# Kernel tuning notes

Hardware: AMD Instinct MI355X
Metric: run time of the kernel (lower is better)

The kernel has to match this reference:

```python
import jax, jax.numpy as jnp
import numpy as np

M = 4  # mixture size of the AttentionStem value embedding

def unfold_windows(a, kh, kw, Hout, Wout):
    # a: [..., Hp, Wp] -> [..., Hout, Wout, kh, kw] (stride-1 sliding windows, cropped)
    rows = []
    for i in range(kh):
        cols = [a[..., i:i + Hout, j:j + Wout] for j in range(kw)]
        rows.append(jnp.stack(cols, axis=-1))
    return jnp.stack(rows, axis=-2)

def attention_stem(x, qw, kw_, vw, emb_a, emb_b, emb_mix, kh, kw, pad):
    # x: [B,Cin,H,W]; qw/kw_: [Cin,Co]; vw: [M,Cin,Co]; emb_a:[Co,kh]; emb_b:[Co,kw]; emb_mix:[M,Co]
    B, Cin, H, W = x.shape
    pl, pr, pt, pb = pad  # F.pad order (left,right,top,bottom)
    xp = jnp.pad(x, ((0, 0), (0, 0), (pt, pb), (pl, pr)))
    Hp, Wp = xp.shape[2], xp.shape[3]
    Hout = min(Hp - kh + 1, H)
    Wout = min(Wp - kw + 1, W)
    q = jnp.einsum('bchw,co->bohw', x[:, :, :Hout, :Wout], qw)       # 1x1 conv query
    k = jnp.einsum('bchw,co->bohw', xp, kw_)                          # 1x1 conv key on padded
    v = jnp.einsum('bchw,mco->mbohw', xp, vw)                         # m 1x1 conv values
    k_win = unfold_windows(k, kh, kw, Hout, Wout)                     # [B,Co,Ho,Wo,kh,kw]
    v_win = unfold_windows(v, kh, kw, Hout, Wout)                     # [M,B,Co,Ho,Wo,kh,kw]
    # mixture relative-position embedding, softmax over mixtures per (kh,kw) offset
    la = emb_mix @ emb_a                                              # [M,kh]
    lb = emb_mix @ emb_b                                              # [M,kw]
    emb = jax.nn.softmax(la[:, :, None] + lb[:, None, :], axis=0)     # [M,kh,kw]
    v_agg = jnp.einsum('mkl,mbohwkl->bohwkl', emb, v_win)             # [B,Co,Ho,Wo,kh,kw]
    K = kh * kw
    scores = jnp.einsum('bohw,bohwkl->bhwkl', q, k_win).reshape(B, Hout, Wout, K)
    attn = jax.nn.softmax(scores, axis=-1).reshape(B, Hout, Wout, kh, kw)
    out = jnp.einsum('bhwkl,bohwkl->bohw', attn, v_agg)               # [B,Co,Ho,Wo]
    return out

def bn_relu(x, g, b):
    # training-mode BatchNorm2d + ReLU
    mu = x.mean(axis=(0, 2, 3), keepdims=True)
    var = x.var(axis=(0, 2, 3), keepdims=True)
    y = (x - mu) * jax.lax.rsqrt(var + 1e-5) * g[None, :, None, None] + b[None, :, None, None]
    return jax.nn.relu(y)

def _params(key):
    ks = jax.random.split(key, 18)
    def w(k, shape):
        return jax.random.normal(k, shape, dtype=jnp.float32) * 0.1
    cfg = [(1, 64, 1, 5), (64, 128, 2, 5), (128, 16, 2, 5)]
    p = {}
    i = 0
    for s, (ci, co, kh, kw) in enumerate(cfg):
        p[f'p{s}_q'] = w(ks[i], (ci, co)); i += 1
        p[f'p{s}_k'] = w(ks[i], (ci, co)); i += 1
        p[f'p{s}_v'] = w(ks[i], (M, ci, co)); i += 1
        p[f'p{s}_ea'] = w(ks[i], (co, kh)); i += 1
        p[f'p{s}_eb'] = w(ks[i], (co, kw)); i += 1
        p[f'p{s}_em'] = w(ks[i], (M, co)); i += 1
        p[f'p{s}_g'] = jnp.ones((co,), jnp.float32)
        p[f'p{s}_b'] = jnp.zeros((co,), jnp.float32)
    return p

def setup_inputs() -> dict:
    key = jax.random.key(0)
    kx, kp = jax.random.split(key)
    inp = {'x': jax.random.normal(kx, (2, 1, 8, 3000), dtype=jnp.float32)}
    inp.update(_params(kp))
    return inp

def reference(x,
              p0_q, p0_k, p0_v, p0_ea, p0_eb, p0_em, p0_g, p0_b,
              p1_q, p1_k, p1_v, p1_ea, p1_eb, p1_em, p1_g, p1_b,
              p2_q, p2_k, p2_v, p2_ea, p2_eb, p2_em, p2_g, p2_b):
    h = attention_stem(x, p0_q, p0_k, p0_v, p0_ea, p0_eb, p0_em, 1, 5, (2, 2, 0, 0))
    h = bn_relu(h, p0_g, p0_b)[:, :, ::2, ::2]                        # MaxPool2d(1,2) == stride-2 subsample
    h = attention_stem(h, p1_q, p1_k, p1_v, p1_ea, p1_eb, p1_em, 2, 5, (2, 2, 1, 1))
    h = bn_relu(h, p1_g, p1_b)[:, :, ::2, ::2]
    h = attention_stem(h, p2_q, p2_k, p2_v, p2_ea, p2_eb, p2_em, 2, 5, (2, 2, 0, 0))
    h = bn_relu(h, p2_g, p2_b)
    B, C, H, W = h.shape
    nW = W // 56                                                       # AvgPool2d((1,56))
    return h[:, :, :, :nW * 56].reshape(B, C, H, nW, 56).mean(-1)
```

## Files before the change

### kernel.cpp

```cpp
#include <hip/hip_runtime.h>
#include <math.h>


#define TPB 256

__global__ void stage0_kernel(const float* __restrict__ x,
                              const float* __restrict__ qw0, const float* __restrict__ kw0,
                              const float* __restrict__ vw0, const float* __restrict__ ea0,
                              const float* __restrict__ eb0, const float* __restrict__ em0,
                              const float* __restrict__ qw1, const float* __restrict__ kw1,
                              const float* __restrict__ vw1, const float* __restrict__ ea1,
                              const float* __restrict__ eb1, const float* __restrict__ em1,
                              const float* __restrict__ qw2, const float* __restrict__ kw2,
                              const float* __restrict__ vw2, const float* __restrict__ ea2,
                              const float* __restrict__ eb2, const float* __restrict__ em2,
                              float* __restrict__ h0raw,
                              float2* __restrict__ part0,
                              float* __restrict__ G,
                              float* __restrict__ Wy,
                              float* __restrict__ embs1g,
                              float* __restrict__ Wcat2) {
    int tid = threadIdx.x;
    int bx = blockIdx.x;
    if (bx >= 94) {
        if (blockIdx.y != 0 || blockIdx.z != 0) return;
        int role = bx - 94;
        __shared__ float la[8], lb[20], embs[40];
        if (role == 0) {
            if (tid < 8) {
                int m = tid / 2, k = tid % 2;
                float s = 0.f;
                for (int o = 0; o < 128; ++o) s += em1[m * 128 + o] * ea1[o * 2 + k];
                la[tid] = s;
            }
            if (tid >= 64 && tid < 84) {
                int r = tid - 64;
                int m = r / 5, l = r % 5;
                float s = 0.f;
                for (int o = 0; o < 128; ++o) s += em1[m * 128 + o] * eb1[o * 5 + l];
                lb[r] = s;
            }
            __syncthreads();
            if (tid < 10) {
                int k = tid / 5, l = tid % 5;
                float lg[4], mx = -1e30f;
                for (int m = 0; m < 4; ++m) {
                    lg[m] = la[m * 2 + k] + lb[m * 5 + l];
                    mx = fmaxf(mx, lg[m]);
                }
                float sum = 0.f;
                for (int m = 0; m < 4; ++m) { lg[m] = expf(lg[m] - mx); sum += lg[m]; }
                float inv = 1.f / sum;
                for (int m = 0; m < 4; ++m) embs[tid * 4 + m] = lg[m] * inv;
            }
            __syncthreads();
            if (tid < 40) embs1g[tid] = embs[tid];
            for (int e = tid; e < 2048; e += 256) {
                int c = e >> 6, c2 = e & 63;
                float s = 0.f;
                for (int o = 0; o < 128; ++o)
                    s = fmaf(qw1[c * 128 + o], kw1[c2 * 128 + o], s);
                G[e] = s;
            }
        } else if (role == 1) {
            for (int e = 2048 + tid; e < 4096; e += 256) {
                int c = e >> 6, c2 = e & 63;
                float s = 0.f;
                for (int o = 0; o < 128; ++o)
                    s = fmaf(qw1[c * 128 + o], kw1[c2 * 128 + o], s);
                G[e] = s;
            }
        } else if (role == 2 || role == 3) {
            int base = (role - 2) * 16384;
            for (int e = base + tid; e < base + 16384; e += 256) {
                int r = e >> 6, c = e & 63;
                int m = r >> 7, o = r & 127;
                Wy[e] = vw1[(m * 64 + c) * 128 + o];
            }
        } else {
            if (tid < 8) {
                int m = tid / 2, k = tid % 2;
                float s = 0.f;
                for (int o = 0; o < 16; ++o) s += em2[m * 16 + o] * ea2[o * 2 + k];
                la[tid] = s;
            }
            if (tid >= 64 && tid < 84) {
                int r = tid - 64;
                int m = r / 5, l = r % 5;
                float s = 0.f;
                for (int o = 0; o < 16; ++o) s += em2[m * 16 + o] * eb2[o * 5 + l];
                lb[r] = s;
            }
            __syncthreads();
            if (tid < 10) {
                int k = tid / 5, l = tid % 5;
                float lg[4], mx = -1e30f;
                for (int m = 0; m < 4; ++m) {
                    lg[m] = la[m * 2 + k] + lb[m * 5 + l];
                    mx = fmaxf(mx, lg[m]);
                }
                float sum = 0.f;
                for (int m = 0; m < 4; ++m) { lg[m] = expf(lg[m] - mx); sum += lg[m]; }
                float inv = 1.f / sum;
                for (int m = 0; m < 4; ++m) embs[tid * 4 + m] = lg[m] * inv;
            }
            __syncthreads();
            int base = (role - 4) * 6144;
            for (int e = base + tid; e < base + 6144; e += 256) {
                int row = e >> 7, c = e & 127;
                float val;
                if (row < 16) {
                    val = qw2[c * 16 + row];
                } else if (row < 32) {
                    val = kw2[c * 16 + (row - 16)];
                } else {
                    int t = (row - 32) >> 4, o = (row - 32) & 15;
                    val = 0.f;
                    for (int m = 0; m < 4; ++m)
                        val += embs[t * 4 + m] * vw2[(m * 128 + c) * 16 + o];
                }
                Wcat2[e] = val;
            }
        }
        return;
    }
    __shared__ float wsh[5][256];
    __shared__ float vsh[320];
    __shared__ float wred[4][20];
    __shared__ float wfin[20];
    __shared__ float la0[4], lb0[20], embs0[20];
    __shared__ float c0s;
    int b = blockIdx.y;
    int oz = blockIdx.z;
    int n0 = bx * 256;
    int n = n0 + tid;
    if (tid < 64) {
        float p = qw0[tid] * kw0[tid];
#pragma unroll
        for (int d = 1; d < 64; d <<= 1) p += __shfl_xor(p, d, 64);
        if (tid == 0) c0s = p;
    }
    if (tid >= 64 && tid < 68) {
        int m = tid - 64;
        float s = 0.f;
        for (int o = 0; o < 64; ++o) s += em0[m * 64 + o] * ea0[o];
        la0[m] = s;
    }
    if (tid >= 128 && tid < 148) {
        int r = tid - 128;
        int m = r / 5, l = r % 5;
        float s = 0.f;
        for (int o = 0; o < 64; ++o) s += em0[m * 64 + o] * eb0[o * 5 + l];
        lb0[m * 5 + l] = s;
    }
    __syncthreads();
    if (tid < 5) {
        float lg[4], mx = -1e30f;
        for (int m = 0; m < 4; ++m) {
            lg[m] = la0[m] + lb0[m * 5 + tid];
            mx = fmaxf(mx, lg[m]);
        }
        float sum = 0.f;
        for (int m = 0; m < 4; ++m) { lg[m] = expf(lg[m] - mx); sum += lg[m]; }
        float inv = 1.f / sum;
        for (int m = 0; m < 4; ++m) embs0[tid * 4 + m] = lg[m] * inv;
    }
    __syncthreads();
    for (int e = tid; e < 320; e += 256) {
        int t = e / 64, o = e - t * 64;
        float s = 0.f;
        for (int m = 0; m < 4; ++m) s += embs0[t * 4 + m] * vw0[m * 64 + o];
        vsh[e] = s;
    }
    __syncthreads();
    float c0 = c0s;
    float warr[5];
    if (n < 24000) {
        int h = n / 3000, w = n - h * 3000;
        const float* xr = x + b * 24000 + h * 3000;
        float xc = xr[w];
        float xs[5], s[5];
#pragma unroll
        for (int t = 0; t < 5; ++t) {
            int col = w + t - 2;
            xs[t] = (col >= 0 && col < 3000) ? xr[col] : 0.f;
            s[t] = c0 * xc * xs[t];
        }
        float mx = s[0];
#pragma unroll
        for (int t = 1; t < 5; ++t) mx = fmaxf(mx, s[t]);
        float sum = 0.f;
#pragma unroll
        for (int t = 0; t < 5; ++t) { s[t] = expf(s[t] - mx); sum += s[t]; }
        float inv = 1.f / sum;
#pragma unroll
        for (int t = 0; t < 5; ++t) warr[t] = s[t] * inv * xs[t];
    } else {
#pragma unroll
        for (int t = 0; t < 5; ++t) warr[t] = 0.f;
    }
#pragma unroll
    for (int t = 0; t < 5; ++t) wsh[t][tid] = warr[t];
    float p[20];
#pragma unroll
    for (int t = 0; t < 5; ++t) p[t] = warr[t];
    {
        int k = 5;
#pragma unroll
        for (int t = 0; t < 5; ++t)
#pragma unroll
            for (int t2 = t; t2 < 5; ++t2) p[k++] = warr[t] * warr[t2];
    }
#pragma unroll
    for (int d = 1; d < 64; d <<= 1)
#pragma unroll
        for (int i = 0; i < 20; ++i) p[i] += __shfl_xor(p[i], d, 64);
    if ((tid & 63) == 0)
#pragma unroll
        for (int i = 0; i < 20; ++i) wred[tid >> 6][i] = p[i];
    __syncthreads();
    if (tid < 20)
        wfin[tid] = wred[0][tid] + wred[1][tid] + wred[2][tid] + wred[3][tid];
    __syncthreads();
    int jq = tid & 63, og = tid >> 6;
    int nq = n0 + jq * 4;
    int h = nq / 3000, w0 = nq - h * 3000;
    bool st = (nq < 24000) && ((h & 1) == 0);
    float wq[5][4];
#pragma unroll
    for (int t = 0; t < 5; ++t)
#pragma unroll
        for (int j = 0; j < 4; ++j) wq[t][j] = wsh[t][jq * 4 + j];
    int obase = oz * 32 + og * 8;
    for (int oi = 0; oi < 8; ++oi) {
        int o = obase + oi;
        float4 v = make_float4(0.f, 0.f, 0.f, 0.f);
#pragma unroll
        for (int t = 0; t < 5; ++t) {
            float vo = vsh[t * 64 + o];
            v.x = fmaf(wq[t][0], vo, v.x);
            v.y = fmaf(wq[t][1], vo, v.y);
            v.z = fmaf(wq[t][2], vo, v.z);
            v.w = fmaf(wq[t][3], vo, v.w);
        }
        if (st) {
            size_t base = ((size_t)b * 64 + o) * 6000 + (h >> 1) * 1500 + (w0 >> 1);
            *(float2*)&h0raw[base] = make_float2(v.x, v.z);
        }
    }
    if (tid < 32) {
        int o = oz * 32 + tid;
        float vt[5];
#pragma unroll
        for (int t = 0; t < 5; ++t) vt[t] = vsh[t * 64 + o];
        float s = 0.f, s2 = 0.f;
#pragma unroll
        for (int t = 0; t < 5; ++t) s = fmaf(vt[t], wfin[t], s);
        int k = 5;
#pragma unroll
        for (int t = 0; t < 5; ++t)
#pragma unroll
            for (int t2 = t; t2 < 5; ++t2) {
                float coef = (t == t2) ? vt[t] * vt[t] : 2.f * vt[t] * vt[t2];
                s2 = fmaf(coef, wfin[k], s2);
                ++k;
            }
        int chunk = b * 94 + bx;
        part0[(size_t)o * 188 + chunk] = make_float2(s, s2);
    }
}

__launch_bounds__(256)
__global__ void stage1_dual_kernel(const float* __restrict__ G,
                                   const float* __restrict__ Wy,
                                   const float* __restrict__ xraw,
                                   const float2* __restrict__ part0,
                                   const float* __restrict__ g0,
                                   const float* __restrict__ b0,
                                   float* __restrict__ attn,
                                   float* __restrict__ ybuf) {
    __shared__ float smem[13696];
    int tid = threadIdx.x;
    int bx = blockIdx.x;
    if (bx < 192) {
        float (*xw)[2][68] = (float(*)[2][68])smem;
        float (*gbuf)[64]  = (float(*)[64])(smem + 8704);
        float (*ssh)[12]   = (float(*)[12])(smem + 12800);
        float* scb = smem + 13568;
        float* sfb = smem + 13632;
        int b = bx / 96;
        int rem = bx % 96;
        int ho = rem / 24, chunk = rem % 24;
        int wo0 = chunk * 64;
        if (tid < 64) {
            double s = 0.0, s2 = 0.0;
            const float2* pp = part0 + (size_t)tid * 188;
            for (int i = 0; i < 188; ++i) { float2 p = pp[i]; s += p.x; s2 += p.y; }
            double mean = s / 48000.0;
            double var = s2 / 48000.0 - mean * mean;
            float rstd = (float)(1.0 / sqrt(var + 1e-5));
            float sc = rstd * g0[tid];
            scb[tid] = sc;
            sfb[tid] = b0[tid] - (float)mean * sc;
        }
        for (int e = tid; e < 4096; e += 256)
            gbuf[e >> 6][e & 63] = G[e];
        __syncthreads();
        for (int e = tid; e < 64 * 136; e += 256) {
            int c = e / 136;
            int r2 = e - c * 136;
            int r = r2 / 68, jj = r2 - r * 68;
            int row = ho - 1 + r;
            int col = wo0 + jj - 2;
            float v = 0.f;
            if (row >= 0 && col >= 0 && col < 1500) {
                float xv = xraw[((size_t)b * 64 + c) * 6000 + row * 1500 + col];
                v = fmaxf(fmaf(xv, scb[c], sfb[c]), 0.f);
            }
            xw[c][r][jj] = v;
        }
        __syncthreads();
        int j = tid & 63, cg = tid >> 6;
        float ul[16];
#pragma unroll
        for (int i = 0; i < 16; ++i) ul[i] = 0.f;
        for (int c = 0; c < 64; ++c) {
            float xv = xw[c][1][j + 2];
            float4 q0 = *(const float4*)&gbuf[c][cg * 16 + 0];
            float4 q1 = *(const float4*)&gbuf[c][cg * 16 + 4];
            float4 q2 = *(const float4*)&gbuf[c][cg * 16 + 8];
            float4 q3 = *(const float4*)&gbuf[c][cg * 16 + 12];
            ul[0]  = fmaf(q0.x, xv, ul[0]);  ul[1]  = fmaf(q0.y, xv, ul[1]);
            ul[2]  = fmaf(q0.z, xv, ul[2]);  ul[3]  = fmaf(q0.w, xv, ul[3]);
            ul[4]  = fmaf(q1.x, xv, ul[4]);  ul[5]  = fmaf(q1.y, xv, ul[5]);
            ul[6]  = fmaf(q1.z, xv, ul[6]);  ul[7]  = fmaf(q1.w, xv, ul[7]);
            ul[8]  = fmaf(q2.x, xv, ul[8]);  ul[9]  = fmaf(q2.y, xv, ul[9]);
            ul[10] = fmaf(q2.z, xv, ul[10]); ul[11] = fmaf(q2.w, xv, ul[11]);
            ul[12] = fmaf(q3.x, xv, ul[12]); ul[13] = fmaf(q3.y, xv, ul[13]);
            ul[14] = fmaf(q3.z, xv, ul[14]); ul[15] = fmaf(q3.w, xv, ul[15]);
        }
        __syncthreads();
#pragma unroll
        for (int i = 0; i < 16; ++i) gbuf[cg * 16 + i][j] = ul[i];
        __syncthreads();
        int t0 = cg, t1 = cg + 4, t2 = cg + 8;
        int dk0 = t0 / 5, dl0 = t0 % 5;
        int dk1 = t1 / 5, dl1 = t1 % 5;
        int dk2 = (t2 < 10) ? 1 : 0, dl2 = (t2 < 10) ? (t2 - 5) : 0;
        float s0 = 0.f, s1 = 0.f, s2v = 0.f;
        for (int c = 0; c < 64; ++c) {
            float uv = gbuf[c][j];
            s0 = fmaf(uv, xw[c][dk0][j + dl0], s0);
            s1 = fmaf(uv, xw[c][dk1][j + dl1], s1);
            if (t2 < 10) s2v = fmaf(uv, xw[c][dk2][j + dl2], s2v);
        }
        ssh[j][t0] = s0;
        ssh[j][t1] = s1;
        if (t2 < 10) ssh[j][t2] = s2v;
        __syncthreads();
        if (tid < 64 && wo0 + tid < 1500) {
            float sc[10];
            float mx = -1e30f;
#pragma unroll
            for (int t = 0; t < 10; ++t) { sc[t] = ssh[tid][t]; mx = fmaxf(mx, sc[t]); }
            float sum = 0.f;
#pragma unroll
            for (int t = 0; t < 10; ++t) { sc[t] = expf(sc[t] - mx); sum += sc[t]; }
            float inv = 1.f / sum;
            int n = ho * 1500 + wo0 + tid;
#pragma unroll
            for (int t = 0; t < 10; ++t)
                attn[((size_t)b * 10 + t) * 6000 + n] = sc[t] * inv;
        }
    } else {
        float (*As)[132] = (float(*)[132])smem;
        float (*Bs)[132] = (float(*)[132])(smem + 4224);
        float* scale = smem + 8448;
        float* shift = smem + 8512;
        int r = bx - 192;
        int b = r / 188;
        int rem = r % 188;
        int mt = rem / 47, nt = rem % 47;
        int m0 = mt * 128, n0 = nt * 128;
        if (tid < 64) {
            double s = 0.0, s2 = 0.0;
            const float2* pp = part0 + (size_t)tid * 188;
            for (int i = 0; i < 188; ++i) { float2 p = pp[i]; s += p.x; s2 += p.y; }
            double mean = s / 48000.0;
            double var = s2 / 48000.0 - mean * mean;
            float rstd = (float)(1.0 / sqrt(var + 1e-5));
            float sc = rstd * g0[tid];
            scale[tid] = sc;
            shift[tid] = b0[tid] - (float)mean * sc;
        }
        __syncthreads();
        float acc[8][8] = {{0.f}};
        int am = tid >> 1, ak = (tid & 1) * 16;
        int bk = tid >> 3, bn = (tid & 7) * 16;
        int tm = tid & 15, tn = tid >> 4;
        for (int k0 = 0; k0 < 64; k0 += 32) {
            {
                const float* Ap = Wy + (size_t)(m0 + am) * 64 + k0 + ak;
#pragma unroll
                for (int q = 0; q < 4; ++q) {
                    float4 v = *(const float4*)(Ap + q * 4);
                    int kk = ak + q * 4;
                    As[kk + 0][am] = v.x;
                    As[kk + 1][am] = v.y;
                    As[kk + 2][am] = v.z;
                    As[kk + 3][am] = v.w;
                }
            }
            {
                int c = k0 + bk;
                float sc = scale[c], sf = shift[c];
                const float* Xp = xraw + ((size_t)b * 64 + c) * 6000 + n0 + bn;
                if (n0 + 128 <= 6000) {
#pragma unroll
                    for (int q = 0; q < 4; ++q) {
                        float4 v = *(const float4*)(Xp + q * 4);
                        v.x = fmaxf(fmaf(v.x, sc, sf), 0.f);
                        v.y = fmaxf(fmaf(v.y, sc, sf), 0.f);
                        v.z = fmaxf(fmaf(v.z, sc, sf), 0.f);
                        v.w = fmaxf(fmaf(v.w, sc, sf), 0.f);
                        *(float4*)&Bs[bk][bn + q * 4] = v;
                    }
                } else {
#pragma unroll
                    for (int q = 0; q < 16; ++q) {
                        int n = n0 + bn + q;
                        Bs[bk][bn + q] = (n < 6000) ? fmaxf(fmaf(Xp[q], sc, sf), 0.f) : 0.f;
                    }
                }
            }
            __syncthreads();
#pragma unroll 8
            for (int k = 0; k < 32; ++k) {
                float4 a0 = *(const float4*)&As[k][tm * 4];
                float4 a1 = *(const float4*)&As[k][64 + tm * 4];
                float4 bb0 = *(const float4*)&Bs[k][tn * 4];
                float4 bb1 = *(const float4*)&Bs[k][64 + tn * 4];
                float av[8] = {a0.x, a0.y, a0.z, a0.w, a1.x, a1.y, a1.z, a1.w};
                float bv[8] = {bb0.x, bb0.y, bb0.z, bb0.w, bb1.x, bb1.y, bb1.z, bb1.w};
#pragma unroll
                for (int i = 0; i < 8; ++i)
#pragma unroll
                    for (int jx = 0; jx < 8; ++jx)
                        acc[i][jx] = fmaf(av[i], bv[jx], acc[i][jx]);
            }
            __syncthreads();
        }
        bool fullN = (n0 + 128 <= 6000);
#pragma unroll
        for (int iq = 0; iq < 2; ++iq) {
            int mb = m0 + iq * 64 + tm * 4;
#pragma unroll
            for (int i = 0; i < 4; ++i) {
                int row = mb + i;
                float* zp = &ybuf[((size_t)b * 512 + row) * 6000];
#pragma unroll
                for (int jq = 0; jq < 2; ++jq) {
                    int nb_ = n0 + jq * 64 + tn * 4;
                    if (fullN) {
                        *(float4*)&zp[nb_] = make_float4(acc[iq * 4 + i][jq * 4 + 0],
                                                         acc[iq * 4 + i][jq * 4 + 1],
                                                         acc[iq * 4 + i][jq * 4 + 2],
                                                         acc[iq * 4 + i][jq * 4 + 3]);
                    } else {
#pragma unroll
                        for (int jj = 0; jj < 4; ++jj)
                            if (nb_ + jj < 6000) zp[nb_ + jj] = acc[iq * 4 + i][jq * 4 + jj];
                    }
                }
            }
        }
    }
}

__global__ void combine1_kernel(const float* __restrict__ y,
                                const float* __restrict__ attn,
                                const float* __restrict__ embs1,
                                float* __restrict__ h1raw,
                                float2* __restrict__ part1) {
    __shared__ float yw[4][2][256];
    __shared__ float embl[40];
    __shared__ float sh[TPB], sh2[TPB];
    int tid = threadIdx.x;
    int bx = blockIdx.x;
    int ho = bx / 6, wc = bx - ho * 6;
    int wo0 = wc * 250;
    int by = blockIdx.y;
    int b = by >> 7, o = by & 127;
    if (tid < 40) embl[tid] = embs1[tid];
    for (int e = tid; e < 4 * 2 * 256; e += 256) {
        int m = e >> 9;
        int rem = e & 511;
        int r = rem >> 8, j = rem & 255;
        int row = ho - 1 + r;
        int col = wo0 - 2 + j;
        float v = 0.f;
        if (j < 254 && row >= 0 && row < 4 && col >= 0 && col < 1500)
            v = y[((size_t)b * 512 + m * 128 + o) * 6000 + row * 1500 + col];
        yw[m][r][j] = v;
    }
    __syncthreads();
    float val = 0.f;
    int wo = wo0 + tid;
    if (tid < 250) {
        int n = ho * 1500 + wo;
        float a[10];
#pragma unroll
        for (int t = 0; t < 10; ++t)
            a[t] = attn[((size_t)b * 10 + t) * 6000 + n];
#pragma unroll
        for (int m = 0; m < 4; ++m) {
#pragma unroll
            for (int dk = 0; dk < 2; ++dk)
#pragma unroll
                for (int dl = 0; dl < 5; ++dl) {
                    int t = dk * 5 + dl;
                    val = fmaf(a[t] * embl[t * 4 + m], yw[m][dk][tid + dl], val);
                }
        }
        if (((ho | wo) & 1) == 0)
            h1raw[((size_t)b * 128 + o) * 1500 + (ho >> 1) * 750 + (wo >> 1)] = val;
    }
    sh[tid] = (tid < 250) ? val : 0.f;
    sh2[tid] = (tid < 250) ? val * val : 0.f;
    __syncthreads();
    for (int st = TPB / 2; st > 0; st >>= 1) {
        if (tid < st) { sh[tid] += sh[tid + st]; sh2[tid] += sh2[tid + st]; }
        __syncthreads();
    }
    if (tid == 0) {
        int chunk = b * 24 + bx;
        part1[(size_t)o * 48 + chunk] = make_float2(sh[0], sh2[0]);
    }
}

__launch_bounds__(256, 4)
__global__ void gemm2_kernel(const float* __restrict__ A,
                             const float* __restrict__ xraw,
                             const float2* __restrict__ part1,
                             const float* __restrict__ g1,
                             const float* __restrict__ b1,
                             float* __restrict__ qk,
                             float* __restrict__ z) {
    const int M = 192, N = 1500, K = 128, twoCo = 32, Mz = 160;
    __shared__ float As[32][132];
    __shared__ float Bs[32][132];
    __shared__ float scale[128], shift[128];
    int tid = threadIdx.x;
    int b = blockIdx.z;
    int m0 = blockIdx.y * 128, n0 = blockIdx.x * 128;
    float acc[8][8] = {{0.f}};
    int am = tid >> 1, ak = (tid & 1) * 16;
    int bk = tid >> 3, bn = (tid & 7) * 16;
    int tm = tid & 15, tn = tid >> 4;
    if (tid < 128) {
        double s = 0.0, s2 = 0.0;
        const float2* pp = part1 + (size_t)tid * 48;
        for (int i = 0; i < 48; ++i) { float2 p = pp[i]; s += p.x; s2 += p.y; }
        double mean = s / 12000.0;
        double var = s2 / 12000.0 - mean * mean;
        float rstd = (float)(1.0 / sqrt(var + 1e-5));
        float sc = rstd * g1[tid];
        scale[tid] = sc;
        shift[tid] = b1[tid] - (float)mean * sc;
    }
    __syncthreads();
    for (int k0 = 0; k0 < K; k0 += 32) {
        {
            int mA = m0 + am;
            const float* Ap = A + (size_t)mA * K + k0 + ak;
#pragma unroll
            for (int q = 0; q < 4; ++q) {
                float4 v = (mA < M) ? *(const float4*)(Ap + q * 4)
                                    : make_float4(0.f, 0.f, 0.f, 0.f);
                int kk = ak + q * 4;
                As[kk + 0][am] = v.x;
                As[kk + 1][am] = v.y;
                As[kk + 2][am] = v.z;
                As[kk + 3][am] = v.w;
            }
        }
        {
            int c = k0 + bk;
            float sc = scale[c], sf = shift[c];
            const float* Xp = xraw + ((size_t)b * K + c) * N + n0 + bn;
            if (n0 + 128 <= N) {
#pragma unroll
                for (int q = 0; q < 4; ++q) {
                    float4 v = *(const float4*)(Xp + q * 4);
                    v.x = fmaxf(fmaf(v.x, sc, sf), 0.f);
                    v.y = fmaxf(fmaf(v.y, sc, sf), 0.f);
                    v.z = fmaxf(fmaf(v.z, sc, sf), 0.f);
                    v.w = fmaxf(fmaf(v.w, sc, sf), 0.f);
                    *(float4*)&Bs[bk][bn + q * 4] = v;
                }
            } else {
#pragma unroll
                for (int q = 0; q < 16; ++q) {
                    int n = n0 + bn + q;
                    Bs[bk][bn + q] = (n < N) ? fmaxf(fmaf(Xp[q], sc, sf), 0.f) : 0.f;
                }
            }
        }
        __syncthreads();
#pragma unroll 8
        for (int k = 0; k < 32; ++k) {
            float4 a0 = *(const float4*)&As[k][tm * 4];
            float4 a1 = *(const float4*)&As[k][64 + tm * 4];
            float4 bb0 = *(const float4*)&Bs[k][tn * 4];
            float4 bb1 = *(const float4*)&Bs[k][64 + tn * 4];
            float av[8] = {a0.x, a0.y, a0.z, a0.w, a1.x, a1.y, a1.z, a1.w};
            float bv[8] = {bb0.x, bb0.y, bb0.z, bb0.w, bb1.x, bb1.y, bb1.z, bb1.w};
#pragma unroll
            for (int i = 0; i < 8; ++i)
#pragma unroll
                for (int jx = 0; jx < 8; ++jx)
                    acc[i][jx] = fmaf(av[i], bv[jx], acc[i][jx]);
        }
        __syncthreads();
    }
    bool fullN = (n0 + 128 <= N);
#pragma unroll
    for (int iq = 0; iq < 2; ++iq) {
        int mb = m0 + iq * 64 + tm * 4;
        if (mb >= M) continue;
        if (mb < twoCo) {
#pragma unroll
            for (int jq = 0; jq < 2; ++jq)
#pragma unroll
                for (int jj = 0; jj < 4; ++jj) {
                    int n = n0 + jq * 64 + tn * 4 + jj;
                    if (n < N) {
                        float4 v = make_float4(acc[iq * 4 + 0][jq * 4 + jj],
                                               acc[iq * 4 + 1][jq * 4 + jj],
                                               acc[iq * 4 + 2][jq * 4 + jj],
                                               acc[iq * 4 + 3][jq * 4 + jj]);
                        *(float4*)&qk[((size_t)b * N + n) * twoCo + mb] = v;
                    }
                }
        } else {
#pragma unroll
            for (int i = 0; i < 4; ++i) {
                int row = mb + i - twoCo;
                float* zp = &z[((size_t)b * Mz + row) * N];
#pragma unroll
                for (int jq = 0; jq < 2; ++jq) {
                    int nb_ = n0 + jq * 64 + tn * 4;
                    if (fullN) {
                        *(float4*)&zp[nb_] = make_float4(acc[iq * 4 + i][jq * 4 + 0],
                                                         acc[iq * 4 + i][jq * 4 + 1],
                                                         acc[iq * 4 + i][jq * 4 + 2],
                                                         acc[iq * 4 + i][jq * 4 + 3]);
                    } else {
#pragma unroll
                        for (int jj = 0; jj < 4; ++jj)
                            if (nb_ + jj < N) zp[nb_ + jj] = acc[iq * 4 + i][jq * 4 + jj];
                    }
                }
            }
        }
    }
}

__global__ void attn_combine2_kernel(const float* __restrict__ qk,
                                     const float* __restrict__ z,
                                     float* __restrict__ out,
                                     float2* __restrict__ part) {
    __shared__ float sh[TPB], sh2[TPB];
    int tid = threadIdx.x;
    int bx = blockIdx.x;
    int by = blockIdx.y;
    int b = by >> 4, o = by & 15;
    int n = bx * 256 + tid;
    float val = 0.f;
    if (n < 750) {
        const float* qp = qk + ((size_t)b * 1500 + n) * 32;
        float q[16];
#pragma unroll
        for (int i = 0; i < 16; i += 4) {
            float4 v = *(const float4*)(qp + i);
            q[i] = v.x; q[i + 1] = v.y; q[i + 2] = v.z; q[i + 3] = v.w;
        }
        float s[10];
        bool valid[10];
        int col[10];
#pragma unroll
        for (int dk = 0; dk < 2; ++dk)
#pragma unroll
            for (int dl = 0; dl < 5; ++dl) {
                int t = dk * 5 + dl;
                int c = n + dl - 2;
                valid[t] = (c >= 0 && c < 750);
                col[t] = dk * 750 + c;
                float sv = 0.f;
                if (valid[t]) {
                    const float* kp = qk + ((size_t)b * 1500 + col[t]) * 32 + 16;
#pragma unroll
                    for (int i = 0; i < 16; i += 4) {
                        float4 k4 = *(const float4*)(kp + i);
                        sv += q[i] * k4.x + q[i + 1] * k4.y + q[i + 2] * k4.z + q[i + 3] * k4.w;
                    }
                }
                s[t] = sv;
            }
        float mx = s[0];
#pragma unroll
        for (int t = 1; t < 10; ++t) mx = fmaxf(mx, s[t]);
        float sum = 0.f;
#pragma unroll
        for (int t = 0; t < 10; ++t) { s[t] = expf(s[t] - mx); sum += s[t]; }
        float inv = 1.f / sum;
#pragma unroll
        for (int t = 0; t < 10; ++t) {
            if (valid[t]) {
                float zv = z[((size_t)b * 160 + t * 16 + o) * 1500 + col[t]];
                val = fmaf(s[t] * inv, zv, val);
            }
        }
        out[((size_t)b * 16 + o) * 750 + n] = val;
    }
    sh[tid] = (n < 750) ? val : 0.f;
    sh2[tid] = (n < 750) ? val * val : 0.f;
    __syncthreads();
    for (int st = TPB / 2; st > 0; st >>= 1) {
        if (tid < st) { sh[tid] += sh[tid + st]; sh2[tid] += sh2[tid + st]; }
        __syncthreads();
    }
    if (tid == 0)
        part[(size_t)o * 6 + b * 3 + bx] = make_float2(sh[0], sh2[0]);
}

__global__ void bn_avg_final_kernel(const float* __restrict__ x,
                                    const float2* __restrict__ part,
                                    const float* __restrict__ g,
                                    const float* __restrict__ bb,
                                    float* __restrict__ out,
                                    int B, int C, int W, int nW, int NCH) {
    int idx = blockIdx.x * blockDim.x + threadIdx.x;
    int N = B * C * nW;
    if (idx >= N) return;
    int j = idx % nW; int r = idx / nW;
    int c = r % C; int b = r / C;
    double s = 0.0, s2 = 0.0;
    for (int i = 0; i < NCH; ++i) {
        float2 p = part[(size_t)c * NCH + i];
        s += p.x; s2 += p.y;
    }
    double cnt = (double)B * W;
    double mean = s / cnt;
    double var = s2 / cnt - mean * mean;
    float rstd = (float)(1.0 / sqrt(var + 1e-5));
    float meanf = (float)mean, gg = g[c], bo = bb[c];
    const float* xb = x + ((long long)b * C + c) * W + j * 56;
    float acc = 0.f;
    for (int i = 0; i < 56; ++i) {
        float yn = (xb[i] - meanf) * rstd * gg + bo;
        acc += fmaxf(yn, 0.f);
    }
    out[idx] = acc * (1.f / 56.f);
}

extern "C" void kernel_launch(void* const* d_in, const int* in_sizes, int n_in,
                              void* d_out, int out_size, void* d_ws, size_t ws_size,
                              hipStream_t stream) {
    const float* x   = (const float*)d_in[0];
    const float* qw0 = (const float*)d_in[1];
    const float* kw0 = (const float*)d_in[2];
    const float* vw0 = (const float*)d_in[3];
    const float* ea0 = (const float*)d_in[4];
    const float* eb0 = (const float*)d_in[5];
    const float* em0 = (const float*)d_in[6];
    const float* g0  = (const float*)d_in[7];
    const float* b0  = (const float*)d_in[8];
    const float* qw1 = (const float*)d_in[9];
    const float* kw1 = (const float*)d_in[10];
    const float* vw1 = (const float*)d_in[11];
    const float* ea1 = (const float*)d_in[12];
    const float* eb1 = (const float*)d_in[13];
    const float* em1 = (const float*)d_in[14];
    const float* g1  = (const float*)d_in[15];
    const float* b1  = (const float*)d_in[16];
    const float* qw2 = (const float*)d_in[17];
    const float* kw2 = (const float*)d_in[18];
    const float* vw2 = (const float*)d_in[19];
    const float* ea2 = (const float*)d_in[20];
    const float* eb2 = (const float*)d_in[21];
    const float* em2 = (const float*)d_in[22];
    const float* g2  = (const float*)d_in[23];
    const float* b2  = (const float*)d_in[24];
    float* outp = (float*)d_out;
    (void)ws_size; (void)in_sizes; (void)n_in; (void)out_size;

    float* ws = (float*)d_ws;
    size_t off = 0;
    auto alloc = [&](size_t n) { float* p = ws + off; off += (n + 63) & ~(size_t)63; return p; };

    float* part0  = alloc(64 * 188 * 2);
    float* h0raw  = alloc(2 * 64 * 6000);
    float* G1     = alloc(64 * 64);
    float* Wy1    = alloc(512 * 64);
    float* embs1  = alloc(64);
    float* Wcat2  = alloc(192 * 128);
    float* attn1  = alloc(2 * 10 * 6000);
    float* ybuf   = alloc(2 * 512 * 6000);
    float* part1  = alloc(128 * 48 * 2);
    float* h1raw  = alloc(2 * 128 * 1500);
    float* qk2    = alloc(2 * 1500 * 32);
    float* z2     = alloc(2 * 160 * 1500);
    float* part2  = alloc(16 * 6 * 2);
    float* s2     = alloc(2 * 16 * 750);

    auto grid = [](int n) { return (n + TPB - 1) / TPB; };

    {
        dim3 g(102, 2, 2);
        stage0_kernel<<<g, TPB, 0, stream>>>(x,
            qw0, kw0, vw0, ea0, eb0, em0,
            qw1, kw1, vw1, ea1, eb1, em1,
            qw2, kw2, vw2, ea2, eb2, em2,
            h0raw, (float2*)part0, G1, Wy1, embs1, Wcat2);
    }
    stage1_dual_kernel<<<568, TPB, 0, stream>>>(G1, Wy1, h0raw,
        (const float2*)part0, g0, b0, attn1, ybuf);
    {
        dim3 g(24, 256);
        combine1_kernel<<<g, TPB, 0, stream>>>(ybuf, attn1, embs1,
            h1raw, (float2*)part1);
    }
    {
        dim3 g(12, 2, 2);
        gemm2_kernel<<<g, TPB, 0, stream>>>(Wcat2, h1raw,
            (const float2*)part1, g1, b1, qk2, z2);
    }
    {
        dim3 g(3, 32);
        attn_combine2_kernel<<<g, TPB, 0, stream>>>(qk2, z2, s2, (float2*)part2);
    }
    bn_avg_final_kernel<<<grid(2 * 16 * 13), TPB, 0, stream>>>(s2,
        (const float2*)part2, g2, b2, outp, 2, 16, 750, 13, 6);
}
```

Before: 275.6 us.

## Split dual-role stage1 kernel into separate attention and GEMM kernels

The fused stage1 kernel, whose blocks branched on index into either attention-score or Y-GEMM work, is split into two kernels launched back to back on the same stream. Each kernel now gets its own register and shared-memory footprint, and the GEMM gets launch_bounds(256,4), which can raise its occupancy. The trade is an extra launch and the loss of concurrency between the attention blocks and the GEMM blocks.

```diff
diff --git a/kernel.cpp b/kernel.cpp
--- a/kernel.cpp
+++ b/kernel.cpp
@@ -270,207 +270,204 @@
     }
 }
 
-__launch_bounds__(256)
-__global__ void stage1_dual_kernel(const float* __restrict__ G,
-                                   const float* __restrict__ Wy,
-                                   const float* __restrict__ xraw,
-                                   const float2* __restrict__ part0,
-                                   const float* __restrict__ g0,
-                                   const float* __restrict__ b0,
-                                   float* __restrict__ attn,
-                                   float* __restrict__ ybuf) {
-    __shared__ float smem[13696];
+__global__ void attn1_kernel(const float* __restrict__ G,
+                             const float* __restrict__ xraw,
+                             const float2* __restrict__ part0,
+                             const float* __restrict__ g0,
+                             const float* __restrict__ b0,
+                             float* __restrict__ attn) {
+    __shared__ float xw[64][2][68];
+    __shared__ float gbuf[64][64];
+    __shared__ float ssh[64][12];
+    __shared__ float scb[64], sfb[64];
     int tid = threadIdx.x;
-    int bx = blockIdx.x;
-    if (bx < 192) {
-        float (*xw)[2][68] = (float(*)[2][68])smem;
-        float (*gbuf)[64]  = (float(*)[64])(smem + 8704);
-        float (*ssh)[12]   = (float(*)[12])(smem + 12800);
-        float* scb = smem + 13568;
-        float* sfb = smem + 13632;
-        int b = bx / 96;
-        int rem = bx % 96;
-        int ho = rem / 24, chunk = rem % 24;
-        int wo0 = chunk * 64;
-        if (tid < 64) {
-            double s = 0.0, s2 = 0.0;
-            const float2* pp = part0 + (size_t)tid * 188;
-            for (int i = 0; i < 188; ++i) { float2 p = pp[i]; s += p.x; s2 += p.y; }
-            double mean = s / 48000.0;
-            double var = s2 / 48000.0 - mean * mean;
-            float rstd = (float)(1.0 / sqrt(var + 1e-5));
-            float sc = rstd * g0[tid];
-            scb[tid] = sc;
-            sfb[tid] = b0[tid] - (float)mean * sc;
-        }
-        for (int e = tid; e < 4096; e += 256)
-            gbuf[e >> 6][e & 63] = G[e];
+    int chunk = blockIdx.x;
+    int ho = blockIdx.y;
+    int b = blockIdx.z;
+    int wo0 = chunk * 64;
+    if (tid < 64) {
+        double s = 0.0, s2 = 0.0;
+        const float2* pp = part0 + (size_t)tid * 188;
+        for (int i = 0; i < 188; ++i) { float2 p = pp[i]; s += p.x; s2 += p.y; }
+        double mean = s / 48000.0;
+        double var = s2 / 48000.0 - mean * mean;
+        float rstd = (float)(1.0 / sqrt(var + 1e-5));
+        float sc = rstd * g0[tid];
+        scb[tid] = sc;
+        sfb[tid] = b0[tid] - (float)mean * sc;
+    }
+    for (int e = tid; e < 4096; e += 256)
+        gbuf[e >> 6][e & 63] = G[e];
+    __syncthreads();
+    for (int e = tid; e < 64 * 136; e += 256) {
+        int c = e / 136;
+        int r2 = e - c * 136;
+        int r = r2 / 68, jj = r2 - r * 68;
+        int row = ho - 1 + r;
+        int col = wo0 + jj - 2;
+        float v = 0.f;
+        if (row >= 0 && col >= 0 && col < 1500) {
+            float xv = xraw[((size_t)b * 64 + c) * 6000 + row * 1500 + col];
+            v = fmaxf(fmaf(xv, scb[c], sfb[c]), 0.f);
+        }
+        xw[c][r][jj] = v;
+    }
+    __syncthreads();
+    int j = tid & 63, cg = tid >> 6;
+    float ul[16];
+#pragma unroll
+    for (int i = 0; i < 16; ++i) ul[i] = 0.f;
+    for (int c = 0; c < 64; ++c) {
+        float xv = xw[c][1][j + 2];
+        float4 q0 = *(const float4*)&gbuf[c][cg * 16 + 0];
+        float4 q1 = *(const float4*)&gbuf[c][cg * 16 + 4];
+        float4 q2 = *(const float4*)&gbuf[c][cg * 16 + 8];
+        float4 q3 = *(const float4*)&gbuf[c][cg * 16 + 12];
+        ul[0]  = fmaf(q0.x, xv, ul[0]);  ul[1]  = fmaf(q0.y, xv, ul[1]);
+        ul[2]  = fmaf(q0.z, xv, ul[2]);  ul[3]  = fmaf(q0.w, xv, ul[3]);
+        ul[4]  = fmaf(q1.x, xv, ul[4]);  ul[5]  = fmaf(q1.y, xv, ul[5]);
+        ul[6]  = fmaf(q1.z, xv, ul[6]);  ul[7]  = fmaf(q1.w, xv, ul[7]);
+        ul[8]  = fmaf(q2.x, xv, ul[8]);  ul[9]  = fmaf(q2.y, xv, ul[9]);
+        ul[10] = fmaf(q2.z, xv, ul[10]); ul[11] = fmaf(q2.w, xv, ul[11]);
+        ul[12] = fmaf(q3.x, xv, ul[12]); ul[13] = fmaf(q3.y, xv, ul[13]);
+        ul[14] = fmaf(q3.z, xv, ul[14]); ul[15] = fmaf(q3.w, xv, ul[15]);
+    }
+    __syncthreads();
+#pragma unroll
+    for (int i = 0; i < 16; ++i) gbuf[cg * 16 + i][j] = ul[i];
+    __syncthreads();
+    int t0 = cg, t1 = cg + 4, t2 = cg + 8;
+    int dk0 = t0 / 5, dl0 = t0 % 5;
+    int dk1 = t1 / 5, dl1 = t1 % 5;
+    int dk2 = (t2 < 10) ? 1 : 0, dl2 = (t2 < 10) ? (t2 - 5) : 0;
+    float s0 = 0.f, s1 = 0.f, s2v = 0.f;
+    for (int c = 0; c < 64; ++c) {
+        float uv = gbuf[c][j];
+        s0 = fmaf(uv, xw[c][dk0][j + dl0], s0);
+        s1 = fmaf(uv, xw[c][dk1][j + dl1], s1);
+        if (t2 < 10) s2v = fmaf(uv, xw[c][dk2][j + dl2], s2v);
+    }
+    ssh[j][t0] = s0;
+    ssh[j][t1] = s1;
+    if (t2 < 10) ssh[j][t2] = s2v;
+    __syncthreads();
+    if (tid < 64 && wo0 + tid < 1500) {
+        float sc[10];
+        float mx = -1e30f;
+#pragma unroll
+        for (int t = 0; t < 10; ++t) { sc[t] = ssh[tid][t]; mx = fmaxf(mx, sc[t]); }
+        float sum = 0.f;
+#pragma unroll
+        for (int t = 0; t < 10; ++t) { sc[t] = expf(sc[t] - mx); sum += sc[t]; }
+        float inv = 1.f / sum;
+        int n = ho * 1500 + wo0 + tid;
+#pragma unroll
+        for (int t = 0; t < 10; ++t)
+            attn[((size_t)b * 10 + t) * 6000 + n] = sc[t] * inv;
+    }
+}
+
+__launch_bounds__(256, 4)
+__global__ void gemm_y_kernel(const float* __restrict__ Wy,
+                              const float* __restrict__ xraw,
+                              const float2* __restrict__ part0,
+                              const float* __restrict__ g0,
+                              const float* __restrict__ b0,
+                              float* __restrict__ ybuf) {
+    __shared__ float As[32][132];
+    __shared__ float Bs[32][132];
+    __shared__ float scale[64], shift[64];
+    int tid = threadIdx.x;
+    int b = blockIdx.z;
+    int m0 = blockIdx.y * 128, n0 = blockIdx.x * 128;
+    if (tid < 64) {
+        double s = 0.0, s2 = 0.0;
+        const float2* pp = part0 + (size_t)tid * 188;
+        for (int i = 0; i < 188; ++i) { float2 p = pp[i]; s += p.x; s2 += p.y; }
+        double mean = s / 48000.0;
+        double var = s2 / 48000.0 - mean * mean;
+        float rstd = (float)(1.0 / sqrt(var + 1e-5));
+        float sc = rstd * g0[tid];
+        scale[tid] = sc;
+        shift[tid] = b0[tid] - (float)mean * sc;
+    }
+    __syncthreads();
+    float acc[8][8] = {{0.f}};
+    int am = tid >> 1, ak = (tid & 1) * 16;
+    int bk = tid >> 3, bn = (tid & 7) * 16;
+    int tm = tid & 15, tn = tid >> 4;
+    for (int k0 = 0; k0 < 64; k0 += 32) {
+        {
+            const float* Ap = Wy + (size_t)(m0 + am) * 64 + k0 + ak;
+#pragma unroll
+            for (int q = 0; q < 4; ++q) {
+                float4 v = *(const float4*)(Ap + q * 4);
+                int kk = ak + q * 4;
+                As[kk + 0][am] = v.x;
+                As[kk + 1][am] = v.y;
+                As[kk + 2][am] = v.z;
+                As[kk + 3][am] = v.w;
+            }
+        }
+        {
+            int c = k0 + bk;
+            float sc = scale[c], sf = shift[c];
+            const float* Xp = xraw + ((size_t)b * 64 + c) * 6000 + n0 + bn;
+            if (n0 + 128 <= 6000) {
+#pragma unroll
+                for (int q = 0; q < 4; ++q) {
+                    float4 v = *(const float4*)(Xp + q * 4);
+                    v.x = fmaxf(fmaf(v.x, sc, sf), 0.f);
+                    v.y = fmaxf(fmaf(v.y, sc, sf), 0.f);
+                    v.z = fmaxf(fmaf(v.z, sc, sf), 0.f);
+                    v.w = fmaxf(fmaf(v.w, sc, sf), 0.f);
+                    *(float4*)&Bs[bk][bn + q * 4] = v;
+                }
+            } else {
+#pragma unroll
+                for (int q = 0; q < 16; ++q) {
+                    int n = n0 + bn + q;
+                    Bs[bk][bn + q] = (n < 6000) ? fmaxf(fmaf(Xp[q], sc, sf), 0.f) : 0.f;
+                }
+            }
+        }
         __syncthreads();
-        for (int e = tid; e < 64 * 136; e += 256) {
-            int c = e / 136;
-            int r2 = e - c * 136;
-            int r = r2 / 68, jj = r2 - r * 68;
-            int row = ho - 1 + r;
-            int col = wo0 + jj - 2;
-            float v = 0.f;
-            if (row >= 0 && col >= 0 && col < 1500) {
-                float xv = xraw[((size_t)b * 64 + c) * 6000 + row * 1500 + col];
-                v = fmaxf(fmaf(xv, scb[c], sfb[c]), 0.f);
-            }
-            xw[c][r][jj] = v;
+#pragma unroll 8
+        for (int k = 0; k < 32; ++k) {
+            float4 a0 = *(const float4*)&As[k][tm * 4];
+            float4 a1 = *(const float4*)&As[k][64 + tm * 4];
+            float4 bb0 = *(const float4*)&Bs[k][tn * 4];
+            float4 bb1 = *(const float4*)&Bs[k][64 + tn * 4];
+            float av[8] = {a0.x, a0.y, a0.z, a0.w, a1.x, a1.y, a1.z, a1.w};
+            float bv[8] = {bb0.x, bb0.y, bb0.z, bb0.w, bb1.x, bb1.y, bb1.z, bb1.w};
+#pragma unroll
+            for (int i = 0; i < 8; ++i)
+#pragma unroll
+                for (int jx = 0; jx < 8; ++jx)
+                    acc[i][jx] = fmaf(av[i], bv[jx], acc[i][jx]);
         }
         __syncthreads();
-        int j = tid & 63, cg = tid >> 6;
-        float ul[16];
-#pragma unroll
-        for (int i = 0; i < 16; ++i) ul[i] = 0.f;
-        for (int c = 0; c < 64; ++c) {
-            float xv = xw[c][1][j + 2];
-            float4 q0 = *(const float4*)&gbuf[c][cg * 16 + 0];
-            float4 q1 = *(const float4*)&gbuf[c][cg * 16 + 4];
-            float4 q2 = *(const float4*)&gbuf[c][cg * 16 + 8];
-            float4 q3 = *(const float4*)&gbuf[c][cg * 16 + 12];
-            ul[0]  = fmaf(q0.x, xv, ul[0]);  ul[1]  = fmaf(q0.y, xv, ul[1]);
-            ul[2]  = fmaf(q0.z, xv, ul[2]);  ul[3]  = fmaf(q0.w, xv, ul[3]);
-            ul[4]  = fmaf(q1.x, xv, ul[4]);  ul[5]  = fmaf(q1.y, xv, ul[5]);
-            ul[6]  = fmaf(q1.z, xv, ul[6]);  ul[7]  = fmaf(q1.w, xv, ul[7]);
-            ul[8]  = fmaf(q2.x, xv, ul[8]);  ul[9]  = fmaf(q2.y, xv, ul[9]);
-            ul[10] = fmaf(q2.z, xv, ul[10]); ul[11] = fmaf(q2.w, xv, ul[11]);
-            ul[12] = fmaf(q3.x, xv, ul[12]); ul[13] = fmaf(q3.y, xv, ul[13]);
-            ul[14] = fmaf(q3.z, xv, ul[14]); ul[15] = fmaf(q3.w, xv, ul[15]);
-        }
-        __syncthreads();
-#pragma unroll
-        for (int i = 0; i < 16; ++i) gbuf[cg * 16 + i][j] = ul[i];
-        __syncthreads();
-        int t0 = cg, t1 = cg + 4, t2 = cg + 8;
-        int dk0 = t0 / 5, dl0 = t0 % 5;
-        int dk1 = t1 / 5, dl1 = t1 % 5;
-        int dk2 = (t2 < 10) ? 1 : 0, dl2 = (t2 < 10) ? (t2 - 5) : 0;
-        float s0 = 0.f, s1 = 0.f, s2v = 0.f;
-        for (int c = 0; c < 64; ++c) {
-            float uv = gbuf[c][j];
-            s0 = fmaf(uv, xw[c][dk0][j + dl0], s0);
-            s1 = fmaf(uv, xw[c][dk1][j + dl1], s1);
-            if (t2 < 10) s2v = fmaf(uv, xw[c][dk2][j + dl2], s2v);
-        }
-        ssh[j][t0] = s0;
-        ssh[j][t1] = s1;
-        if (t2 < 10) ssh[j][t2] = s2v;
-        __syncthreads();
-        if (tid < 64 && wo0 + tid < 1500) {
-            float sc[10];
-            float mx = -1e30f;
-#pragma unroll
-            for (int t = 0; t < 10; ++t) { sc[t] = ssh[tid][t]; mx = fmaxf(mx, sc[t]); }
-            float sum = 0.f;
-#pragma unroll
-            for (int t = 0; t < 10; ++t) { sc[t] = expf(sc[t] - mx); sum += sc[t]; }
-            float inv = 1.f / sum;
-            int n = ho * 1500 + wo0 + tid;
-#pragma unroll
-            for (int t = 0; t < 10; ++t)
-                attn[((size_t)b * 10 + t) * 6000 + n] = sc[t] * inv;
-        }
-    } else {
-        float (*As)[132] = (float(*)[132])smem;
-        float (*Bs)[132] = (float(*)[132])(smem + 4224);
-        float* scale = smem + 8448;
-        float* shift = smem + 8512;
-        int r = bx - 192;
-        int b = r / 188;
-        int rem = r % 188;
-        int mt = rem / 47, nt = rem % 47;
-        int m0 = mt * 128, n0 = nt * 128;
-        if (tid < 64) {
-            double s = 0.0, s2 = 0.0;
-            const float2* pp = part0 + (size_t)tid * 188;
-            for (int i = 0; i < 188; ++i) { float2 p = pp[i]; s += p.x; s2 += p.y; }
-            double mean = s / 48000.0;
-            double var = s2 / 48000.0 - mean * mean;
-            float rstd = (float)(1.0 / sqrt(var + 1e-5));
-            float sc = rstd * g0[tid];
-            scale[tid] = sc;
-            shift[tid] = b0[tid] - (float)mean * sc;
-        }
-        __syncthreads();
-        float acc[8][8] = {{0.f}};
-        int am = tid >> 1, ak = (tid & 1) * 16;
-        int bk = tid >> 3, bn = (tid & 7) * 16;
-        int tm = tid & 15, tn = tid >> 4;
-        for (int k0 = 0; k0 < 64; k0 += 32) {
-            {
-                const float* Ap = Wy + (size_t)(m0 + am) * 64 + k0 + ak;
-#pragma unroll
-                for (int q = 0; q < 4; ++q) {
-                    float4 v = *(const float4*)(Ap + q * 4);
-                    int kk = ak + q * 4;
-                    As[kk + 0][am] = v.x;
-                    As[kk + 1][am] = v.y;
-                    As[kk + 2][am] = v.z;
-                    As[kk + 3][am] = v.w;
-                }
-            }
-            {
-                int c = k0 + bk;
-                float sc = scale[c], sf = shift[c];
-                const float* Xp = xraw + ((size_t)b * 64 + c) * 6000 + n0 + bn;
-                if (n0 + 128 <= 6000) {
-#pragma unroll
-                    for (int q = 0; q < 4; ++q) {
-                        float4 v = *(const float4*)(Xp + q * 4);
-                        v.x = fmaxf(fmaf(v.x, sc, sf), 0.f);
-                        v.y = fmaxf(fmaf(v.y, sc, sf), 0.f);
-                        v.z = fmaxf(fmaf(v.z, sc, sf), 0.f);
-                        v.w = fmaxf(fmaf(v.w, sc, sf), 0.f);
-                        *(float4*)&Bs[bk][bn + q * 4] = v;
-                    }
+    }
+    bool fullN = (n0 + 128 <= 6000);
+#pragma unroll
+    for (int iq = 0; iq < 2; ++iq) {
+        int mb = m0 + iq * 64 + tm * 4;
+#pragma unroll
+        for (int i = 0; i < 4; ++i) {
+            int row = mb + i;
+            float* zp = &ybuf[((size_t)b * 512 + row) * 6000];
+#pragma unroll
+            for (int jq = 0; jq < 2; ++jq) {
+                int nb_ = n0 + jq * 64 + tn * 4;
+                if (fullN) {
+                    *(float4*)&zp[nb_] = make_float4(acc[iq * 4 + i][jq * 4 + 0],
+                                                     acc[iq * 4 + i][jq * 4 + 1],
+                                                     acc[iq * 4 + i][jq * 4 + 2],
+                                                     acc[iq * 4 + i][jq * 4 + 3]);
                 } else {
 #pragma unroll
-                    for (int q = 0; q < 16; ++q) {
-                        int n = n0 + bn + q;
-                        Bs[bk][bn + q] = (n < 6000) ? fmaxf(fmaf(Xp[q], sc, sf), 0.f) : 0.f;
-                    }
-                }
-            }
-            __syncthreads();
-#pragma unroll 8
-            for (int k = 0; k < 32; ++k) {
-                float4 a0 = *(const float4*)&As[k][tm * 4];
-                float4 a1 = *(const float4*)&As[k][64 + tm * 4];
-                float4 bb0 = *(const float4*)&Bs[k][tn * 4];
-                float4 bb1 = *(const float4*)&Bs[k][64 + tn * 4];
-                float av[8] = {a0.x, a0.y, a0.z, a0.w, a1.x, a1.y, a1.z, a1.w};
-                float bv[8] = {bb0.x, bb0.y, bb0.z, bb0.w, bb1.x, bb1.y, bb1.z, bb1.w};
-#pragma unroll
-                for (int i = 0; i < 8; ++i)
-#pragma unroll
-                    for (int jx = 0; jx < 8; ++jx)
-                        acc[i][jx] = fmaf(av[i], bv[jx], acc[i][jx]);
-            }
-            __syncthreads();
-        }
-        bool fullN = (n0 + 128 <= 6000);
-#pragma unroll
-        for (int iq = 0; iq < 2; ++iq) {
-            int mb = m0 + iq * 64 + tm * 4;
-#pragma unroll
-            for (int i = 0; i < 4; ++i) {
-                int row = mb + i;
-                float* zp = &ybuf[((size_t)b * 512 + row) * 6000];
-#pragma unroll
-                for (int jq = 0; jq < 2; ++jq) {
-                    int nb_ = n0 + jq * 64 + tn * 4;
-                    if (fullN) {
-                        *(float4*)&zp[nb_] = make_float4(acc[iq * 4 + i][jq * 4 + 0],
-                                                         acc[iq * 4 + i][jq * 4 + 1],
-                                                         acc[iq * 4 + i][jq * 4 + 2],
-                                                         acc[iq * 4 + i][jq * 4 + 3]);
-                    } else {
-#pragma unroll
-                        for (int jj = 0; jj < 4; ++jj)
-                            if (nb_ + jj < 6000) zp[nb_ + jj] = acc[iq * 4 + i][jq * 4 + jj];
-                    }
+                    for (int jj = 0; jj < 4; ++jj)
+                        if (nb_ + jj < 6000) zp[nb_ + jj] = acc[iq * 4 + i][jq * 4 + jj];
                 }
             }
         }
@@ -824,8 +821,16 @@
             qw2, kw2, vw2, ea2, eb2, em2,
             h0raw, (float2*)part0, G1, Wy1, embs1, Wcat2);
     }
-    stage1_dual_kernel<<<568, TPB, 0, stream>>>(G1, Wy1, h0raw,
-        (const float2*)part0, g0, b0, attn1, ybuf);
+    {
+        dim3 g(24, 4, 2);
+        attn1_kernel<<<g, TPB, 0, stream>>>(G1, h0raw, (const float2*)part0,
+            g0, b0, attn1);
+    }
+    {
+        dim3 g(47, 4, 2);
+        gemm_y_kernel<<<g, TPB, 0, stream>>>(Wy1, h0raw, (const float2*)part0,
+            g0, b0, ybuf);
+    }
     {
         dim3 g(24, 256);
         combine1_kernel<<<g, TPB, 0, stream>>>(ybuf, attn1, embs1,
```

Result: slower. 281.9 us (+2.3%).
